# Performance work log

Hardware: AMD Instinct MI355X
Metric: run time of the kernel (lower is better)

## Reference

```python
import jax, jax.numpy as jnp
import numpy as np

B, S, E, H, R = 512, 50, 128, 8, 32
D = E // H  # depth per head
USERS, ITEMS, ALLSEQ, NCLASS = 50000, 20000, 20000, 5


def setup_inputs() -> dict:
    key = jax.random.key(0)
    ks = jax.random.split(key, 20)
    n = lambda k, shp, s=0.05: jax.random.normal(k, shp, dtype=jnp.float32) * s
    return {
        "user": jax.random.randint(ks[0], (B,), 0, USERS),
        "item": jax.random.randint(ks[1], (B,), 0, ITEMS),
        "neighbor": jax.random.randint(ks[2], (B, S), 0, USERS),
        "seq": jax.random.randint(ks[3], (B, S), 0, ALLSEQ),
        "user_emb_table": n(ks[4], (USERS, E)),
        "item_emb_table": n(ks[5], (ITEMS, E)),
        "user_item_LCU": n(ks[6], (ALLSEQ, R, E), 0.01),
        "item_user_LCU": n(ks[7], (ALLSEQ, R, E), 0.01),
        "wq": n(ks[8], (E, E)), "bq": jnp.zeros((E,), jnp.float32),
        "wk": n(ks[9], (E, E)), "bk": jnp.zeros((E,), jnp.float32),
        "wv": n(ks[10], (E, E)), "bv": jnp.zeros((E,), jnp.float32),
        "wo": n(ks[11], (E, E)), "bo": jnp.zeros((E,), jnp.float32),
        "fc_w": n(ks[12], (R, NCLASS)), "fc_b": jnp.zeros((NCLASS,), jnp.float32),
    }


def _forward(user, item, neighbor, seq,
             user_emb_table, item_emb_table, user_item_LCU, item_user_LCU,
             wq, bq, wk, bk, wv, bv, wo, bo, fc_w, fc_b):
    user_emb = user_emb_table[user]            # [B,E]
    neighbor_emb = user_emb_table[neighbor]    # [B,S,E]
    item_emb = item_emb_table[item]            # [B,E]
    weight = (neighbor > 0).astype(jnp.float32)  # [B,S] padding mask (1=real)

    # ---- single-query multi-head attention (use_attention=True) ----
    q = (user_emb @ wq + bq).reshape(B, H, D)                       # [B,H,D]
    k = (neighbor_emb @ wk + bk).reshape(B, S, H, D).transpose(0, 2, 1, 3)  # [B,H,S,D]
    v = (neighbor_emb @ wv + bv).reshape(B, S, H, D).transpose(0, 2, 1, 3)  # [B,H,S,D]
    logits = jnp.einsum('bhd,bhsd->bhs', q, k) / jnp.sqrt(jnp.float32(D))
    logits = logits + (1.0 - weight)[:, None, :] * (-1e9)           # mask padding
    attn = jax.nn.softmax(logits, axis=-1)                          # [B,H,S]
    ctx = attn[..., None] * v                                       # [B,H,S,D]
    ctx = ctx.transpose(0, 2, 1, 3).reshape(B, S, E)                # [B,S,E]
    neighbor_emb = ctx @ wo + bo                                    # [B,S,E]

    # ---- region embedding ----
    K_ui = user_item_LCU[seq]   # [B,S,R,E]
    K_iu = item_user_LCU[seq]   # [B,S,R,E]
    neighbor_profile = jnp.einsum('bsre,bse->bsr', K_iu, neighbor_emb)  # [B,S,R]
    item_profile = jnp.einsum('bsre,be->bsr', K_ui, item_emb)          # [B,S,R]
    neighbor_rating = neighbor_profile * item_profile * weight[:, :, None]
    user_rating_vector = jnp.max(neighbor_rating, axis=1)              # [B,R]

    # ---- rating classifier ----
    return jax.nn.softmax(user_rating_vector @ fc_w + fc_b, axis=-1)   # [B,NCLASS]


def reference(user, item, neighbor, seq,
              user_emb_table, item_emb_table, user_item_LCU, item_user_LCU,
              wq, bq, wk, bk, wv, bv, wo, bo, fc_w, fc_b):
    return _forward(user, item, neighbor, seq,
                    user_emb_table, item_emb_table, user_item_LCU, item_user_LCU,
                    wq, bq, wk, bk, wv, bv, wo, bo, fc_w, fc_b)
```

## Files before the change

kernel.cpp:

```cpp
#include <hip/hip_runtime.h>
#include <math.h>

#define BB 512
#define SS 50
#define EE 128
#define HH 8
#define RR 32
#define NC 5
#define NSEQ 20000
#define NBS (BB*SS)
#define LDK 136

typedef __attribute__((ext_vector_type(8))) __bf16 bf16x8;
typedef __attribute__((ext_vector_type(4))) float f32x4;
typedef __attribute__((ext_vector_type(4))) unsigned short us4;

__device__ __forceinline__ unsigned short f2bf(float f) {
    unsigned int u = __float_as_uint(f);
    unsigned int r = (u + 0x7fffu + ((u >> 16) & 1u)) >> 16;
    return (unsigned short)r;
}
__device__ __forceinline__ float dot4v(const f32x4& a, const float4& b) {
    return a[0]*b.x + a[1]*b.y + a[2]*b.z + a[3]*b.w;
}

__global__ __launch_bounds__(256) void prep_kernel(const float* __restrict__ wv,
                                                   const float* __restrict__ wo,
                                                   const float* __restrict__ wq,
                                                   unsigned short* __restrict__ wvT,
                                                   unsigned short* __restrict__ woT,
                                                   unsigned short* __restrict__ wqT,
                                                   const int* __restrict__ seq,
                                                   int* __restrict__ hist) {
    const int bid = blockIdx.x, t = threadIdx.x;
    if (bid < 128) {
        const int n = bid;
        if (t < 128) {
            wvT[n*EE + t] = f2bf(wv[t*EE + n]);
            wqT[n*EE + t] = f2bf(wq[t*EE + n]);
        } else {
            woT[n*EE + (t - 128)] = f2bf(wo[(t - 128)*EE + n]);
        }
    } else {
        const int i = (bid - 128) * 256 + t;
        if (i < NBS) atomicAdd(&hist[seq[i]], 1);
    }
}

__global__ __launch_bounds__(1024) void scan_kernel(int* __restrict__ hist,
                                                    int* __restrict__ hstart) {
    const int t = threadIdx.x;
    const int CH = 20;
    const int base = t * CH;
    int loc[CH];
    int s = 0;
    #pragma unroll
    for (int i = 0; i < CH; ++i) {
        int idx = base + i;
        int v = (idx < NSEQ) ? hist[idx] : 0;
        loc[i] = s; s += v;
    }
    const int lane = t & 63, w = t >> 6;
    int incl = s;
    #pragma unroll
    for (int off = 1; off < 64; off <<= 1) {
        int n = __shfl_up(incl, off);
        if (lane >= off) incl += n;
    }
    __shared__ int wsum[16];
    if (lane == 63) wsum[w] = incl;
    __syncthreads();
    if (t == 0) {
        int acc = 0;
        #pragma unroll
        for (int k = 0; k < 16; ++k) { int v = wsum[k]; wsum[k] = acc; acc += v; }
    }
    __syncthreads();
    const int excl = incl - s + wsum[w];
    #pragma unroll
    for (int i = 0; i < CH; ++i) {
        int idx = base + i;
        if (idx < NSEQ) {
            int e = excl + loc[i];
            hist[idx] = e;
            hstart[idx] = e;
        }
    }
    if (t == 0) hstart[NSEQ] = NBS;
}

__global__ __launch_bounds__(256) void scatter_kernel(const int* __restrict__ seq,
                                                      int* __restrict__ hist,
                                                      int* __restrict__ perm) {
    int i = blockIdx.x * 256 + threadIdx.x;
    if (i < NBS) {
        int pos = atomicAdd(&hist[seq[i]], 1);
        perm[pos] = i;
    }
}

__global__ __launch_bounds__(256) void qkv_kernel(
    const int* __restrict__ user,
    const float* __restrict__ uet,
    const unsigned short* __restrict__ wqT, const float* __restrict__ bq,
    const float* __restrict__ wk, const float* __restrict__ bk,
    unsigned short* __restrict__ qkvT_ws, float* __restrict__ qkb_ws)
{
    __shared__ unsigned short ueA[64*LDK];
    __shared__ float Qlds[64][EE];

    const int tile = blockIdx.x;
    const int t = threadIdx.x;

    for (int idx = t; idx < 64*32; idx += 256) {
        int r = idx >> 5, g = idx & 31;
        float4 v = ((const float4*)(uet + (size_t)user[tile*64 + r]*EE))[g];
        us4 o; o.x = f2bf(v.x); o.y = f2bf(v.y); o.z = f2bf(v.z); o.w = f2bf(v.w);
        *(us4*)&ueA[r*LDK + g*4] = o;
    }
    __syncthreads();

    const int w    = t >> 6;
    const int l    = t & 63;
    const int lrow = l & 15;
    const int kg   = l >> 4;

    bf16x8 a0 = *(const bf16x8*)&ueA[(w*16 + lrow)*LDK +  0 + kg*8];
    bf16x8 a1 = *(const bf16x8*)&ueA[(w*16 + lrow)*LDK + 32 + kg*8];
    bf16x8 a2 = *(const bf16x8*)&ueA[(w*16 + lrow)*LDK + 64 + kg*8];
    bf16x8 a3 = *(const bf16x8*)&ueA[(w*16 + lrow)*LDK + 96 + kg*8];

    #pragma unroll
    for (int nt = 0; nt < 8; ++nt) {
        const unsigned short* bp = wqT + (nt*16 + lrow)*EE + kg*8;
        bf16x8 b0 = *(const bf16x8*)&bp[0];
        bf16x8 b1 = *(const bf16x8*)&bp[32];
        bf16x8 b2 = *(const bf16x8*)&bp[64];
        bf16x8 b3 = *(const bf16x8*)&bp[96];
        f32x4 c = {0.f, 0.f, 0.f, 0.f};
        c = __builtin_amdgcn_mfma_f32_16x16x32_bf16(a0, b0, c, 0, 0, 0);
        c = __builtin_amdgcn_mfma_f32_16x16x32_bf16(a1, b1, c, 0, 0, 0);
        c = __builtin_amdgcn_mfma_f32_16x16x32_bf16(a2, b2, c, 0, 0, 0);
        c = __builtin_amdgcn_mfma_f32_16x16x32_bf16(a3, b3, c, 0, 0, 0);
        const int col = nt*16 + lrow;
        const float bqc = bq[col];
        #pragma unroll
        for (int rg = 0; rg < 4; ++rg) {
            const int row = w*16 + kg*4 + rg;
            Qlds[row][col] = c[rg] + bqc;
        }
    }
    __syncthreads();

    {
        const int e = t >> 1, h0 = (t & 1) * 4;
        float wkreg[4][16];
        #pragma unroll
        for (int j = 0; j < 4; ++j)
            #pragma unroll
            for (int d = 0; d < 16; ++d)
                wkreg[j][d] = wk[e*EE + (h0 + j)*16 + d];

        for (int b = 0; b < 64; ++b) {
            #pragma unroll
            for (int j = 0; j < 4; ++j) {
                const float4* q4 = (const float4*)&Qlds[b][(h0 + j)*16];
                float acc = 0.f;
                #pragma unroll
                for (int d4 = 0; d4 < 4; ++d4) {
                    float4 q = q4[d4];
                    acc += q.x*wkreg[j][d4*4+0] + q.y*wkreg[j][d4*4+1]
                         + q.z*wkreg[j][d4*4+2] + q.w*wkreg[j][d4*4+3];
                }
                qkvT_ws[(((size_t)(tile*64 + b))*16 + (h0 + j))*EE + e] = f2bf(acc);
            }
        }
    }

    if (t < 64) {
        const int b = t;
        #pragma unroll
        for (int h = 0; h < HH; ++h) {
            float acc = 0.f;
            #pragma unroll
            for (int d = 0; d < 16; ++d)
                acc = fmaf(Qlds[b][h*16 + d], bk[h*16 + d], acc);
            qkb_ws[(size_t)(tile*64 + b)*HH + h] = acc;
        }
    }
}

__global__ __launch_bounds__(256, 4) void attn_kernel(
    const int* __restrict__ neighbor,
    const float* __restrict__ uet,
    const unsigned short* __restrict__ qkvT_ws, const float* __restrict__ qkb_ws,
    const float* __restrict__ bv, const float* __restrict__ bo,
    const unsigned short* __restrict__ wvT, const unsigned short* __restrict__ woT,
    float* __restrict__ ws_ne2)
{
    __shared__ unsigned short kA[64*LDK];
    __shared__ float attn_s[HH][64];
    __shared__ float maskadd[64];

    const int b = blockIdx.x;
    const int t = threadIdx.x;

    if (t < 64) maskadd[t] = (t < SS && neighbor[b*SS + t] > 0) ? 0.f : -1e9f;
    for (int idx = t; idx < SS*32; idx += 256) {
        int s = idx >> 5, g = idx & 31;
        float4 v = ((const float4*)(uet + (size_t)neighbor[b*SS + s]*EE))[g];
        us4 o; o.x = f2bf(v.x); o.y = f2bf(v.y); o.z = f2bf(v.z); o.w = f2bf(v.w);
        *(us4*)&kA[s*LDK + g*4] = o;
    }
    for (int idx = t; idx < 14*LDK; idx += 256) kA[50*LDK + idx] = 0;
    __syncthreads();

    const int w    = t >> 6;
    const int l    = t & 63;
    const int lrow = l & 15;
    const int kg   = l >> 4;

    bf16x8 a0 = *(const bf16x8*)&kA[(w*16 + lrow)*LDK +  0 + kg*8];
    bf16x8 a1 = *(const bf16x8*)&kA[(w*16 + lrow)*LDK + 32 + kg*8];
    bf16x8 a2 = *(const bf16x8*)&kA[(w*16 + lrow)*LDK + 64 + kg*8];
    bf16x8 a3 = *(const bf16x8*)&kA[(w*16 + lrow)*LDK + 96 + kg*8];

    {
        const unsigned short* bp = qkvT_ws + ((size_t)b*16 + lrow)*EE + kg*8;
        bf16x8 b0 = *(const bf16x8*)&bp[0];
        bf16x8 b1 = *(const bf16x8*)&bp[32];
        bf16x8 b2 = *(const bf16x8*)&bp[64];
        bf16x8 b3 = *(const bf16x8*)&bp[96];
        f32x4 c = {0.f, 0.f, 0.f, 0.f};
        c = __builtin_amdgcn_mfma_f32_16x16x32_bf16(a0, b0, c, 0, 0, 0);
        c = __builtin_amdgcn_mfma_f32_16x16x32_bf16(a1, b1, c, 0, 0, 0);
        c = __builtin_amdgcn_mfma_f32_16x16x32_bf16(a2, b2, c, 0, 0, 0);
        c = __builtin_amdgcn_mfma_f32_16x16x32_bf16(a3, b3, c, 0, 0, 0);
        const int h = lrow;
        if (h < HH) {
            const float qkbv = qkb_ws[(size_t)b*HH + h];
            #pragma unroll
            for (int rg = 0; rg < 4; ++rg) {
                const int row = w*16 + kg*4 + rg;
                attn_s[h][row] = (c[rg] + qkbv) * 0.25f + maskadd[row];
            }
        }
    }
    __syncthreads();

    if (t < 64) {
        int h = t >> 3, ll = t & 7;
        float mx = -3e38f;
        #pragma unroll
        for (int i = 0; i < 7; ++i) { int s = i*8 + ll; if (s < SS) mx = fmaxf(mx, attn_s[h][s]); }
        mx = fmaxf(mx, __shfl_xor(mx, 1));
        mx = fmaxf(mx, __shfl_xor(mx, 2));
        mx = fmaxf(mx, __shfl_xor(mx, 4));
        float ev[7]; float sm_ = 0.f;
        #pragma unroll
        for (int i = 0; i < 7; ++i) {
            int s = i*8 + ll; ev[i] = 0.f;
            if (s < SS) { ev[i] = expf(attn_s[h][s] - mx); sm_ += ev[i]; }
        }
        sm_ += __shfl_xor(sm_, 1);
        sm_ += __shfl_xor(sm_, 2);
        sm_ += __shfl_xor(sm_, 4);
        float inv = 1.f / sm_;
        #pragma unroll
        for (int i = 0; i < 7; ++i) { int s = i*8 + ll; if (s < SS) attn_s[h][s] = ev[i] * inv; }
    }
    __syncthreads();

    f32x4 acc[8];
    #pragma unroll
    for (int nt = 0; nt < 8; ++nt) {
        const unsigned short* bp = wvT + (nt*16 + lrow)*EE + kg*8;
        bf16x8 b0 = *(const bf16x8*)&bp[0];
        bf16x8 b1 = *(const bf16x8*)&bp[32];
        bf16x8 b2 = *(const bf16x8*)&bp[64];
        bf16x8 b3 = *(const bf16x8*)&bp[96];
        f32x4 c = {0.f, 0.f, 0.f, 0.f};
        c = __builtin_amdgcn_mfma_f32_16x16x32_bf16(a0, b0, c, 0, 0, 0);
        c = __builtin_amdgcn_mfma_f32_16x16x32_bf16(a1, b1, c, 0, 0, 0);
        c = __builtin_amdgcn_mfma_f32_16x16x32_bf16(a2, b2, c, 0, 0, 0);
        c = __builtin_amdgcn_mfma_f32_16x16x32_bf16(a3, b3, c, 0, 0, 0);
        acc[nt] = c;
    }
    #pragma unroll
    for (int nt = 0; nt < 8; ++nt) {
        const int col = nt*16 + lrow;
        const float bvc = bv[col];
        #pragma unroll
        for (int rg = 0; rg < 4; ++rg) {
            const int row = w*16 + kg*4 + rg;
            const float av = (row < SS) ? attn_s[nt][row] : 0.f;
            kA[row*LDK + col] = f2bf((acc[nt][rg] + bvc) * av);
        }
    }
    __syncthreads();

    bf16x8 c0 = *(const bf16x8*)&kA[(w*16 + lrow)*LDK +  0 + kg*8];
    bf16x8 c1 = *(const bf16x8*)&kA[(w*16 + lrow)*LDK + 32 + kg*8];
    bf16x8 c2 = *(const bf16x8*)&kA[(w*16 + lrow)*LDK + 64 + kg*8];
    bf16x8 c3 = *(const bf16x8*)&kA[(w*16 + lrow)*LDK + 96 + kg*8];

    #pragma unroll
    for (int nt = 0; nt < 8; ++nt) {
        const unsigned short* bp = woT + (nt*16 + lrow)*EE + kg*8;
        bf16x8 b0 = *(const bf16x8*)&bp[0];
        bf16x8 b1 = *(const bf16x8*)&bp[32];
        bf16x8 b2 = *(const bf16x8*)&bp[64];
        bf16x8 b3 = *(const bf16x8*)&bp[96];
        f32x4 c = {0.f, 0.f, 0.f, 0.f};
        c = __builtin_amdgcn_mfma_f32_16x16x32_bf16(c0, b0, c, 0, 0, 0);
        c = __builtin_amdgcn_mfma_f32_16x16x32_bf16(c1, b1, c, 0, 0, 0);
        c = __builtin_amdgcn_mfma_f32_16x16x32_bf16(c2, b2, c, 0, 0, 0);
        c = __builtin_amdgcn_mfma_f32_16x16x32_bf16(c3, b3, c, 0, 0, 0);
        const int col = nt*16 + lrow;
        const float boc = bo[col];
        #pragma unroll
        for (int rg = 0; rg < 4; ++rg) {
            const int row = w*16 + kg*4 + rg;
            if (row < SS)
                ws_ne2[((size_t)b*SS + row)*EE + col] = c[rg] + boc;
        }
    }
}

__global__ __launch_bounds__(256, 6) void region_kernel(
    const int* __restrict__ neighbor, const int* __restrict__ item,
    const float* __restrict__ ui_lcu, const float* __restrict__ iu_lcu,
    const float* __restrict__ iet, const float* __restrict__ ws_ne2,
    const int* __restrict__ hstart, const int* __restrict__ perm,
    float* __restrict__ ws_rating)
{
    const int j = blockIdx.x;
    const int start = hstart[j];
    const int end   = hstart[j + 1];
    if (start >= end) return;

    const int t = threadIdx.x;
    const int r = t >> 3, l = t & 7;

    const f32x4* kiu_g = (const f32x4*)(iu_lcu + ((size_t)j*RR + r)*EE);
    const f32x4* kui_g = (const f32x4*)(ui_lcu + ((size_t)j*RR + r)*EE);
    f32x4 kiu_r[4], kui_r[4];
    #pragma unroll
    for (int i = 0; i < 4; ++i) {
        kiu_r[i] = __builtin_nontemporal_load(&kiu_g[l + 8*i]);
        kui_r[i] = __builtin_nontemporal_load(&kui_g[l + 8*i]);
    }

    for (int o = start; o < end; ++o) {
        const int bs = perm[o];
        const int b  = (unsigned)bs / SS;
        const float4* n4 = (const float4*)(ws_ne2 + (size_t)bs*EE);
        const float4* i4 = (const float4*)(iet + (size_t)item[b]*EE);

        float np_ = 0.f, ip_ = 0.f;
        #pragma unroll
        for (int i = 0; i < 4; ++i) {
            int c = l + 8*i;
            np_ += dot4v(kiu_r[i], n4[c]);
            ip_ += dot4v(kui_r[i], i4[c]);
        }
        np_ += __shfl_xor(np_, 1); np_ += __shfl_xor(np_, 2); np_ += __shfl_xor(np_, 4);
        ip_ += __shfl_xor(ip_, 1); ip_ += __shfl_xor(ip_, 2); ip_ += __shfl_xor(ip_, 4);

        const float w = (neighbor[bs] > 0) ? 1.f : 0.f;
        if (l == 0) ws_rating[(size_t)bs*RR + r] = np_ * ip_ * w;
    }
}

__global__ __launch_bounds__(256) void head_kernel(
    const float* __restrict__ ws_rating,
    const float* __restrict__ fc_w, const float* __restrict__ fc_b,
    float* __restrict__ out)
{
    __shared__ float part[8][RR];
    __shared__ float urv[RR];
    __shared__ float lg[NC];
    const int b = blockIdx.x, t = threadIdx.x;
    const int r = t & 31, sub = t >> 5;

    float m = -3e38f;
    for (int s = sub; s < SS; s += 8)
        m = fmaxf(m, ws_rating[((size_t)b*SS + s)*RR + r]);
    part[sub][r] = m;
    __syncthreads();
    if (t < RR) {
        float mm = part[0][t];
        #pragma unroll
        for (int k = 1; k < 8; ++k) mm = fmaxf(mm, part[k][t]);
        urv[t] = mm;
    }
    __syncthreads();
    if (t < NC) {
        float acc = fc_b[t];
        #pragma unroll
        for (int rr = 0; rr < RR; ++rr) acc = fmaf(urv[rr], fc_w[rr*NC + t], acc);
        lg[t] = acc;
    }
    __syncthreads();
    if (t < NC) {
        float mx = lg[0];
        #pragma unroll
        for (int c = 1; c < NC; ++c) mx = fmaxf(mx, lg[c]);
        float sm = 0.f;
        #pragma unroll
        for (int c = 0; c < NC; ++c) sm += expf(lg[c] - mx);
        out[b*NC + t] = expf(lg[t] - mx) / sm;
    }
}

extern "C" void kernel_launch(void* const* d_in, const int* in_sizes, int n_in,
                              void* d_out, int out_size, void* d_ws, size_t ws_size,
                              hipStream_t stream) {
    const int*   user     = (const int*)d_in[0];
    const int*   item     = (const int*)d_in[1];
    const int*   neighbor = (const int*)d_in[2];
    const int*   seq      = (const int*)d_in[3];
    const float* uet      = (const float*)d_in[4];
    const float* iet      = (const float*)d_in[5];
    const float* ui_lcu   = (const float*)d_in[6];
    const float* iu_lcu   = (const float*)d_in[7];
    const float* wq = (const float*)d_in[8];   const float* bq = (const float*)d_in[9];
    const float* wk = (const float*)d_in[10];  const float* bk = (const float*)d_in[11];
    const float* wv = (const float*)d_in[12];  const float* bv = (const float*)d_in[13];
    const float* wo = (const float*)d_in[14];  const float* bo = (const float*)d_in[15];
    const float* fcw = (const float*)d_in[16]; const float* fcb = (const float*)d_in[17];

    float* ws = (float*)d_ws;
    float* ws_ne2    = ws;
    float* ws_rating = ws_ne2 + (size_t)BB*SS*EE;
    float* qkb_ws    = ws_rating + (size_t)BB*SS*RR;
    unsigned short* wvT = (unsigned short*)(qkb_ws + (size_t)BB*HH);
    unsigned short* woT = wvT + EE*EE;
    unsigned short* wqT = woT + EE*EE;
    unsigned short* qkvT_ws = wqT + EE*EE;
    int*   hist      = (int*)(qkvT_ws + (size_t)BB*16*EE);
    int*   hstart    = hist + NSEQ;
    int*   perm      = hstart + NSEQ + 1;
    float* out = (float*)d_out;

    hipMemsetAsync(hist, 0, NSEQ * sizeof(int), stream);
    hipLaunchKernelGGL(prep_kernel, dim3(128 + (NBS + 255)/256), dim3(256), 0, stream,
                       wv, wo, wq, wvT, woT, wqT, seq, hist);
    hipLaunchKernelGGL(qkv_kernel, dim3(8), dim3(256), 0, stream,
                       user, uet, wqT, bq, wk, bk, qkvT_ws, qkb_ws);
    hipLaunchKernelGGL(scan_kernel, dim3(1), dim3(1024), 0, stream, hist, hstart);
    hipLaunchKernelGGL(scatter_kernel, dim3((NBS + 255)/256), dim3(256), 0, stream,
                       seq, hist, perm);

    hipLaunchKernelGGL(attn_kernel, dim3(BB), dim3(256), 0, stream,
                       neighbor, uet, qkvT_ws, qkb_ws, bv, bo, wvT, woT, ws_ne2);

    hipLaunchKernelGGL(region_kernel, dim3(NSEQ), dim3(256), 0, stream,
                       neighbor, item, ui_lcu, iu_lcu, iet, ws_ne2, hstart, perm, ws_rating);

    hipLaunchKernelGGL(head_kernel, dim3(BB), dim3(256), 0, stream,
                       ws_rating, fcw, fcb, out);
}
```

Baseline: 198.9 us.

## Split region work and overlap item-profile pass with attention in a fused grid

The item-profile dot products (K_ui·item_emb) move out of the region kernel into a fused launch. In that launch every 8th block runs attention for one batch row and the other blocks compute item profiles for 4 seq ids each, so the LCU streaming runs alongside attention. Attention now uses 1024 threads per block, with each wave handling two output column tiles. The later np_kernel reads only iu_lcu plus a stored item-profile buffer. Separately, the Q·Wk projection in qkv_kernel moves to MFMA, and scatter precomputes a permuted item index. The cost is an extra NBS×R float buffer written and read back, plus more launch complexity.

```diff
diff --git a/kernel.cpp b/kernel.cpp
--- a/kernel.cpp
+++ b/kernel.cpp
@@ -10,6 +10,8 @@
 #define NSEQ 20000
 #define NBS (BB*SS)
 #define LDK 136
+#define NIPB 5000
+#define GRIDF 5715
 
 typedef __attribute__((ext_vector_type(8))) __bf16 bf16x8;
 typedef __attribute__((ext_vector_type(4))) float f32x4;
@@ -90,12 +92,15 @@
 }
 
 __global__ __launch_bounds__(256) void scatter_kernel(const int* __restrict__ seq,
+                                                      const int* __restrict__ item,
                                                       int* __restrict__ hist,
-                                                      int* __restrict__ perm) {
+                                                      int* __restrict__ perm,
+                                                      int* __restrict__ pitem) {
     int i = blockIdx.x * 256 + threadIdx.x;
     if (i < NBS) {
         int pos = atomicAdd(&hist[seq[i]], 1);
-        perm[pos] = i;
+        perm[pos]  = i;
+        pitem[pos] = item[(unsigned)i / SS];
     }
 }
 
@@ -107,7 +112,7 @@
     unsigned short* __restrict__ qkvT_ws, float* __restrict__ qkb_ws)
 {
     __shared__ unsigned short ueA[64*LDK];
-    __shared__ float Qlds[64][EE];
+    __shared__ float Qlds[64][132];
 
     const int tile = blockIdx.x;
     const int t = threadIdx.x;
@@ -125,57 +130,31 @@
     const int lrow = l & 15;
     const int kg   = l >> 4;
 
-    bf16x8 a0 = *(const bf16x8*)&ueA[(w*16 + lrow)*LDK +  0 + kg*8];
-    bf16x8 a1 = *(const bf16x8*)&ueA[(w*16 + lrow)*LDK + 32 + kg*8];
-    bf16x8 a2 = *(const bf16x8*)&ueA[(w*16 + lrow)*LDK + 64 + kg*8];
-    bf16x8 a3 = *(const bf16x8*)&ueA[(w*16 + lrow)*LDK + 96 + kg*8];
-
-    #pragma unroll
-    for (int nt = 0; nt < 8; ++nt) {
-        const unsigned short* bp = wqT + (nt*16 + lrow)*EE + kg*8;
-        bf16x8 b0 = *(const bf16x8*)&bp[0];
-        bf16x8 b1 = *(const bf16x8*)&bp[32];
-        bf16x8 b2 = *(const bf16x8*)&bp[64];
-        bf16x8 b3 = *(const bf16x8*)&bp[96];
-        f32x4 c = {0.f, 0.f, 0.f, 0.f};
-        c = __builtin_amdgcn_mfma_f32_16x16x32_bf16(a0, b0, c, 0, 0, 0);
-        c = __builtin_amdgcn_mfma_f32_16x16x32_bf16(a1, b1, c, 0, 0, 0);
-        c = __builtin_amdgcn_mfma_f32_16x16x32_bf16(a2, b2, c, 0, 0, 0);
-        c = __builtin_amdgcn_mfma_f32_16x16x32_bf16(a3, b3, c, 0, 0, 0);
-        const int col = nt*16 + lrow;
-        const float bqc = bq[col];
-        #pragma unroll
-        for (int rg = 0; rg < 4; ++rg) {
-            const int row = w*16 + kg*4 + rg;
-            Qlds[row][col] = c[rg] + bqc;
-        }
-    }
-    __syncthreads();
-
     {
-        const int e = t >> 1, h0 = (t & 1) * 4;
-        float wkreg[4][16];
-        #pragma unroll
-        for (int j = 0; j < 4; ++j)
-            #pragma unroll
-            for (int d = 0; d < 16; ++d)
-                wkreg[j][d] = wk[e*EE + (h0 + j)*16 + d];
-
-        for (int b = 0; b < 64; ++b) {
-            #pragma unroll
-            for (int j = 0; j < 4; ++j) {
-                const float4* q4 = (const float4*)&Qlds[b][(h0 + j)*16];
-                float acc = 0.f;
-                #pragma unroll
-                for (int d4 = 0; d4 < 4; ++d4) {
-                    float4 q = q4[d4];
-                    acc += q.x*wkreg[j][d4*4+0] + q.y*wkreg[j][d4*4+1]
-                         + q.z*wkreg[j][d4*4+2] + q.w*wkreg[j][d4*4+3];
-                }
-                qkvT_ws[(((size_t)(tile*64 + b))*16 + (h0 + j))*EE + e] = f2bf(acc);
-            }
-        }
-    }
+        bf16x8 a0 = *(const bf16x8*)&ueA[(w*16 + lrow)*LDK +  0 + kg*8];
+        bf16x8 a1 = *(const bf16x8*)&ueA[(w*16 + lrow)*LDK + 32 + kg*8];
+        bf16x8 a2 = *(const bf16x8*)&ueA[(w*16 + lrow)*LDK + 64 + kg*8];
+        bf16x8 a3 = *(const bf16x8*)&ueA[(w*16 + lrow)*LDK + 96 + kg*8];
+        #pragma unroll
+        for (int nt = 0; nt < 8; ++nt) {
+            const unsigned short* bp = wqT + (nt*16 + lrow)*EE + kg*8;
+            bf16x8 b0 = *(const bf16x8*)&bp[0];
+            bf16x8 b1 = *(const bf16x8*)&bp[32];
+            bf16x8 b2 = *(const bf16x8*)&bp[64];
+            bf16x8 b3 = *(const bf16x8*)&bp[96];
+            f32x4 c = {0.f, 0.f, 0.f, 0.f};
+            c = __builtin_amdgcn_mfma_f32_16x16x32_bf16(a0, b0, c, 0, 0, 0);
+            c = __builtin_amdgcn_mfma_f32_16x16x32_bf16(a1, b1, c, 0, 0, 0);
+            c = __builtin_amdgcn_mfma_f32_16x16x32_bf16(a2, b2, c, 0, 0, 0);
+            c = __builtin_amdgcn_mfma_f32_16x16x32_bf16(a3, b3, c, 0, 0, 0);
+            const int col = nt*16 + lrow;
+            const float bqc = bq[col];
+            #pragma unroll
+            for (int rg = 0; rg < 4; ++rg)
+                Qlds[w*16 + kg*4 + rg][col] = c[rg] + bqc;
+        }
+    }
+    __syncthreads();
 
     if (t < 64) {
         const int b = t;
@@ -188,44 +167,122 @@
             qkb_ws[(size_t)(tile*64 + b)*HH + h] = acc;
         }
     }
-}
-
-__global__ __launch_bounds__(256, 4) void attn_kernel(
+
+    for (int idx = t; idx < 64*8*EE/4; idx += 256) {
+        const int b = idx >> 8;
+        const int rem = idx & 255;
+        const int h = 8 + (rem >> 5);
+        const int c4 = rem & 31;
+        us4 z = {0, 0, 0, 0};
+        *(us4*)&qkvT_ws[(((size_t)(tile*64 + b))*16 + h)*EE + c4*4] = z;
+    }
+
+    for (int p = 0; p < 64; ++p) {
+        const int h = p >> 3, et = p & 7;
+        bf16x8 af, bf_;
+        if (kg < 2) {
+            #pragma unroll
+            for (int j = 0; j < 8; ++j) {
+                af[j] = (__bf16)0.0f;
+            }
+            #pragma unroll
+            for (int j = 0; j < 8; ++j)
+                ((unsigned short*)&af)[j] = f2bf(Qlds[w*16 + lrow][h*16 + kg*8 + j]);
+            const float* wkp = wk + (size_t)(et*16 + lrow)*EE + h*16 + kg*8;
+            #pragma unroll
+            for (int j = 0; j < 8; ++j)
+                ((unsigned short*)&bf_)[j] = f2bf(wkp[j]);
+        } else {
+            #pragma unroll
+            for (int j = 0; j < 8; ++j) {
+                ((unsigned short*)&af)[j] = 0;
+                ((unsigned short*)&bf_)[j] = 0;
+            }
+        }
+        f32x4 c = {0.f, 0.f, 0.f, 0.f};
+        c = __builtin_amdgcn_mfma_f32_16x16x32_bf16(af, bf_, c, 0, 0, 0);
+        const int e = et*16 + lrow;
+        #pragma unroll
+        for (int rg = 0; rg < 4; ++rg) {
+            const int b = w*16 + kg*4 + rg;
+            qkvT_ws[(((size_t)(tile*64 + b))*16 + h)*EE + e] = f2bf(c[rg]);
+        }
+    }
+}
+
+__global__ __launch_bounds__(1024, 8) void fused_kernel(
     const int* __restrict__ neighbor,
     const float* __restrict__ uet,
     const unsigned short* __restrict__ qkvT_ws, const float* __restrict__ qkb_ws,
     const float* __restrict__ bv, const float* __restrict__ bo,
     const unsigned short* __restrict__ wvT, const unsigned short* __restrict__ woT,
-    float* __restrict__ ws_ne2)
+    const float* __restrict__ ui_lcu, const float* __restrict__ iet,
+    const int* __restrict__ hstart, const int* __restrict__ perm,
+    const int* __restrict__ pitem,
+    float* __restrict__ ws_ne2, float* __restrict__ ws_ip)
 {
     __shared__ unsigned short kA[64*LDK];
     __shared__ float attn_s[HH][64];
     __shared__ float maskadd[64];
 
-    const int b = blockIdx.x;
+    const int bid = blockIdx.x;
     const int t = threadIdx.x;
 
-    if (t < 64) maskadd[t] = (t < SS && neighbor[b*SS + t] > 0) ? 0.f : -1e9f;
-    for (int idx = t; idx < SS*32; idx += 256) {
+    if ((bid & 7) != 0) {
+        const int ip_idx = bid - (bid >> 3) - 1;
+        const int jq = ip_idx*4 + (t >> 8);
+        const int t2 = t & 255, r = t2 >> 3, l = t2 & 7;
+        const int start = hstart[jq];
+        const int end   = hstart[jq + 1];
+        if (start >= end) return;
+
+        const f32x4* kui = (const f32x4*)(ui_lcu + ((size_t)jq*RR + r)*EE);
+        f32x4 k0 = __builtin_nontemporal_load(&kui[l]);
+        f32x4 k1 = __builtin_nontemporal_load(&kui[l + 8]);
+        f32x4 k2 = __builtin_nontemporal_load(&kui[l + 16]);
+        f32x4 k3 = __builtin_nontemporal_load(&kui[l + 24]);
+
+        for (int o = start; o < end; ++o) {
+            const float4* i4 = (const float4*)(iet + (size_t)pitem[o]*EE);
+            float acc = dot4v(k0, i4[l]) + dot4v(k1, i4[l+8])
+                      + dot4v(k2, i4[l+16]) + dot4v(k3, i4[l+24]);
+            acc += __shfl_xor(acc, 1); acc += __shfl_xor(acc, 2); acc += __shfl_xor(acc, 4);
+            if (l == 0) ws_ip[(size_t)perm[o]*RR + r] = acc;
+        }
+        return;
+    }
+
+    const int q = bid >> 3;
+    if (q >= BB) return;
+    const int b = q;
+
+    if (t >= 128 && t < 192) {
+        const int s = t - 128;
+        const bool real = (s < SS) && (neighbor[b*SS + s] > 0);
+        maskadd[s] = real ? 0.f : -1e9f;
+    }
+    for (int idx = t; idx < SS*32; idx += 1024) {
         int s = idx >> 5, g = idx & 31;
         float4 v = ((const float4*)(uet + (size_t)neighbor[b*SS + s]*EE))[g];
         us4 o; o.x = f2bf(v.x); o.y = f2bf(v.y); o.z = f2bf(v.z); o.w = f2bf(v.w);
         *(us4*)&kA[s*LDK + g*4] = o;
     }
-    for (int idx = t; idx < 14*LDK; idx += 256) kA[50*LDK + idx] = 0;
+    for (int idx = t; idx < 14*LDK; idx += 1024) kA[50*LDK + idx] = 0;
     __syncthreads();
 
     const int w    = t >> 6;
     const int l    = t & 63;
     const int lrow = l & 15;
     const int kg   = l >> 4;
-
-    bf16x8 a0 = *(const bf16x8*)&kA[(w*16 + lrow)*LDK +  0 + kg*8];
-    bf16x8 a1 = *(const bf16x8*)&kA[(w*16 + lrow)*LDK + 32 + kg*8];
-    bf16x8 a2 = *(const bf16x8*)&kA[(w*16 + lrow)*LDK + 64 + kg*8];
-    bf16x8 a3 = *(const bf16x8*)&kA[(w*16 + lrow)*LDK + 96 + kg*8];
-
-    {
+    const int rt   = w & 3;
+    const int np   = w >> 2;
+
+    bf16x8 a0 = *(const bf16x8*)&kA[(rt*16 + lrow)*LDK +  0 + kg*8];
+    bf16x8 a1 = *(const bf16x8*)&kA[(rt*16 + lrow)*LDK + 32 + kg*8];
+    bf16x8 a2 = *(const bf16x8*)&kA[(rt*16 + lrow)*LDK + 64 + kg*8];
+    bf16x8 a3 = *(const bf16x8*)&kA[(rt*16 + lrow)*LDK + 96 + kg*8];
+
+    if (np == 0) {
         const unsigned short* bp = qkvT_ws + ((size_t)b*16 + lrow)*EE + kg*8;
         bf16x8 b0 = *(const bf16x8*)&bp[0];
         bf16x8 b1 = *(const bf16x8*)&bp[32];
@@ -241,7 +298,7 @@
             const float qkbv = qkb_ws[(size_t)b*HH + h];
             #pragma unroll
             for (int rg = 0; rg < 4; ++rg) {
-                const int row = w*16 + kg*4 + rg;
+                const int row = rt*16 + kg*4 + rg;
                 attn_s[h][row] = (c[rg] + qkbv) * 0.25f + maskadd[row];
             }
         }
@@ -271,9 +328,9 @@
     }
     __syncthreads();
 
-    f32x4 acc[8];
     #pragma unroll
-    for (int nt = 0; nt < 8; ++nt) {
+    for (int qq = 0; qq < 2; ++qq) {
+        const int nt = np*2 + qq;
         const unsigned short* bp = wvT + (nt*16 + lrow)*EE + kg*8;
         bf16x8 b0 = *(const bf16x8*)&bp[0];
         bf16x8 b1 = *(const bf16x8*)&bp[32];
@@ -284,28 +341,25 @@
         c = __builtin_amdgcn_mfma_f32_16x16x32_bf16(a1, b1, c, 0, 0, 0);
         c = __builtin_amdgcn_mfma_f32_16x16x32_bf16(a2, b2, c, 0, 0, 0);
         c = __builtin_amdgcn_mfma_f32_16x16x32_bf16(a3, b3, c, 0, 0, 0);
-        acc[nt] = c;
-    }
-    #pragma unroll
-    for (int nt = 0; nt < 8; ++nt) {
         const int col = nt*16 + lrow;
         const float bvc = bv[col];
         #pragma unroll
         for (int rg = 0; rg < 4; ++rg) {
-            const int row = w*16 + kg*4 + rg;
+            const int row = rt*16 + kg*4 + rg;
             const float av = (row < SS) ? attn_s[nt][row] : 0.f;
-            kA[row*LDK + col] = f2bf((acc[nt][rg] + bvc) * av);
-        }
-    }
-    __syncthreads();
-
-    bf16x8 c0 = *(const bf16x8*)&kA[(w*16 + lrow)*LDK +  0 + kg*8];
-    bf16x8 c1 = *(const bf16x8*)&kA[(w*16 + lrow)*LDK + 32 + kg*8];
-    bf16x8 c2 = *(const bf16x8*)&kA[(w*16 + lrow)*LDK + 64 + kg*8];
-    bf16x8 c3 = *(const bf16x8*)&kA[(w*16 + lrow)*LDK + 96 + kg*8];
+            kA[row*LDK + col] = f2bf((c[rg] + bvc) * av);
+        }
+    }
+    __syncthreads();
+
+    bf16x8 c0 = *(const bf16x8*)&kA[(rt*16 + lrow)*LDK +  0 + kg*8];
+    bf16x8 c1 = *(const bf16x8*)&kA[(rt*16 + lrow)*LDK + 32 + kg*8];
+    bf16x8 c2 = *(const bf16x8*)&kA[(rt*16 + lrow)*LDK + 64 + kg*8];
+    bf16x8 c3 = *(const bf16x8*)&kA[(rt*16 + lrow)*LDK + 96 + kg*8];
 
     #pragma unroll
-    for (int nt = 0; nt < 8; ++nt) {
+    for (int qq = 0; qq < 2; ++qq) {
+        const int nt = np*2 + qq;
         const unsigned short* bp = woT + (nt*16 + lrow)*EE + kg*8;
         bf16x8 b0 = *(const bf16x8*)&bp[0];
         bf16x8 b1 = *(const bf16x8*)&bp[32];
@@ -320,17 +374,17 @@
         const float boc = bo[col];
         #pragma unroll
         for (int rg = 0; rg < 4; ++rg) {
-            const int row = w*16 + kg*4 + rg;
+            const int row = rt*16 + kg*4 + rg;
             if (row < SS)
                 ws_ne2[((size_t)b*SS + row)*EE + col] = c[rg] + boc;
         }
     }
 }
 
-__global__ __launch_bounds__(256, 6) void region_kernel(
-    const int* __restrict__ neighbor, const int* __restrict__ item,
-    const float* __restrict__ ui_lcu, const float* __restrict__ iu_lcu,
-    const float* __restrict__ iet, const float* __restrict__ ws_ne2,
+__global__ __launch_bounds__(256, 6) void np_kernel(
+    const int* __restrict__ neighbor,
+    const float* __restrict__ iu_lcu,
+    const float* __restrict__ ws_ne2, const float* __restrict__ ws_ip,
     const int* __restrict__ hstart, const int* __restrict__ perm,
     float* __restrict__ ws_rating)
 {
@@ -342,33 +396,22 @@
     const int t = threadIdx.x;
     const int r = t >> 3, l = t & 7;
 
-    const f32x4* kiu_g = (const f32x4*)(iu_lcu + ((size_t)j*RR + r)*EE);
-    const f32x4* kui_g = (const f32x4*)(ui_lcu + ((size_t)j*RR + r)*EE);
-    f32x4 kiu_r[4], kui_r[4];
-    #pragma unroll
-    for (int i = 0; i < 4; ++i) {
-        kiu_r[i] = __builtin_nontemporal_load(&kiu_g[l + 8*i]);
-        kui_r[i] = __builtin_nontemporal_load(&kui_g[l + 8*i]);
-    }
+    const f32x4* kiu = (const f32x4*)(iu_lcu + ((size_t)j*RR + r)*EE);
+    f32x4 k0 = __builtin_nontemporal_load(&kiu[l]);
+    f32x4 k1 = __builtin_nontemporal_load(&kiu[l + 8]);
+    f32x4 k2 = __builtin_nontemporal_load(&kiu[l + 16]);
+    f32x4 k3 = __builtin_nontemporal_load(&kiu[l + 24]);
 
     for (int o = start; o < end; ++o) {
         const int bs = perm[o];
-        const int b  = (unsigned)bs / SS;
         const float4* n4 = (const float4*)(ws_ne2 + (size_t)bs*EE);
-        const float4* i4 = (const float4*)(iet + (size_t)item[b]*EE);
-
-        float np_ = 0.f, ip_ = 0.f;
-        #pragma unroll
-        for (int i = 0; i < 4; ++i) {
-            int c = l + 8*i;
-            np_ += dot4v(kiu_r[i], n4[c]);
-            ip_ += dot4v(kui_r[i], i4[c]);
-        }
-        np_ += __shfl_xor(np_, 1); np_ += __shfl_xor(np_, 2); np_ += __shfl_xor(np_, 4);
-        ip_ += __shfl_xor(ip_, 1); ip_ += __shfl_xor(ip_, 2); ip_ += __shfl_xor(ip_, 4);
-
-        const float w = (neighbor[bs] > 0) ? 1.f : 0.f;
-        if (l == 0) ws_rating[(size_t)bs*RR + r] = np_ * ip_ * w;
+        float acc = dot4v(k0, n4[l]) + dot4v(k1, n4[l+8])
+                  + dot4v(k2, n4[l+16]) + dot4v(k3, n4[l+24]);
+        acc += __shfl_xor(acc, 1); acc += __shfl_xor(acc, 2); acc += __shfl_xor(acc, 4);
+        if (l == 0) {
+            const float wgt = (neighbor[bs] > 0) ? 1.f : 0.f;
+            ws_rating[(size_t)bs*RR + r] = acc * ws_ip[(size_t)bs*RR + r] * wgt;
+        }
     }
 }
 
@@ -433,7 +476,8 @@
     float* ws = (float*)d_ws;
     float* ws_ne2    = ws;
     float* ws_rating = ws_ne2 + (size_t)BB*SS*EE;
-    float* qkb_ws    = ws_rating + (size_t)BB*SS*RR;
+    float* ws_ip     = ws_rating + (size_t)NBS*RR;
+    float* qkb_ws    = ws_ip + (size_t)NBS*RR;
     unsigned short* wvT = (unsigned short*)(qkb_ws + (size_t)BB*HH);
     unsigned short* woT = wvT + EE*EE;
     unsigned short* wqT = woT + EE*EE;
@@ -441,22 +485,24 @@
     int*   hist      = (int*)(qkvT_ws + (size_t)BB*16*EE);
     int*   hstart    = hist + NSEQ;
     int*   perm      = hstart + NSEQ + 1;
+    int*   pitem     = perm + NBS;
     float* out = (float*)d_out;
 
     hipMemsetAsync(hist, 0, NSEQ * sizeof(int), stream);
     hipLaunchKernelGGL(prep_kernel, dim3(128 + (NBS + 255)/256), dim3(256), 0, stream,
                        wv, wo, wq, wvT, woT, wqT, seq, hist);
+    hipLaunchKernelGGL(scan_kernel, dim3(1), dim3(1024), 0, stream, hist, hstart);
+    hipLaunchKernelGGL(scatter_kernel, dim3((NBS + 255)/256), dim3(256), 0, stream,
+                       seq, item, hist, perm, pitem);
     hipLaunchKernelGGL(qkv_kernel, dim3(8), dim3(256), 0, stream,
                        user, uet, wqT, bq, wk, bk, qkvT_ws, qkb_ws);
-    hipLaunchKernelGGL(scan_kernel, dim3(1), dim3(1024), 0, stream, hist, hstart);
-    hipLaunchKernelGGL(scatter_kernel, dim3((NBS + 255)/256), dim3(256), 0, stream,
-                       seq, hist, perm);
-
-    hipLaunchKernelGGL(attn_kernel, dim3(BB), dim3(256), 0, stream,
-                       neighbor, uet, qkvT_ws, qkb_ws, bv, bo, wvT, woT, ws_ne2);
-
-    hipLaunchKernelGGL(region_kernel, dim3(NSEQ), dim3(256), 0, stream,
-                       neighbor, item, ui_lcu, iu_lcu, iet, ws_ne2, hstart, perm, ws_rating);
+
+    hipLaunchKernelGGL(fused_kernel, dim3(GRIDF), dim3(1024), 0, stream,
+                       neighbor, uet, qkvT_ws, qkb_ws, bv, bo, wvT, woT,
+                       ui_lcu, iet, hstart, perm, pitem, ws_ne2, ws_ip);
+
+    hipLaunchKernelGGL(np_kernel, dim3(NSEQ), dim3(256), 0, stream,
+                       neighbor, iu_lcu, ws_ne2, ws_ip, hstart, perm, ws_rating);
 
     hipLaunchKernelGGL(head_kernel, dim3(BB), dim3(256), 0, stream,
                        ws_rating, fcw, fcb, out);
```

After: 279.4 us. 40.5% more time.
